# Kernel tuning notes

Measured on AMD Instinct MI355X. Metric: run time of the kernel, lower is better.

The kernel has to match this reference:

```python
import jax, jax.numpy as jnp
import numpy as np

B, SQ, HIDDEN = 2, 2048, 2048
HEADS, GROUPS, KVC = 16, 4, 128
HPG = HEADS // GROUPS          # heads per group
LAYER_INDEX = 1
SCALE = KVC ** -0.5            # attention_softmax_scale_power = 0.5


def setup_inputs() -> dict:
    key = jax.random.key(0)
    k1, k2, k3, k4 = jax.random.split(key, 4)
    return {
        "x": jax.random.normal(k1, (B, SQ, HIDDEN), jnp.float32),
        "w_q": jax.random.normal(k2, (HIDDEN, HEADS * KVC), jnp.float32) * 0.02,
        "w_kv": jax.random.normal(k3, (HIDDEN, 2 * GROUPS * KVC), jnp.float32) * 0.02,
        "w_dense": jax.random.normal(k4, (HEADS * KVC, HIDDEN), jnp.float32) * 0.02,
    }


def reference(x, w_q, w_kv, w_dense):
    b, sq, _ = x.shape
    sk = sq
    # QKV projections
    q = jnp.einsum("bsh,he->bse", x, w_q).reshape(b, sq, GROUPS, HPG, KVC)
    kv = jnp.einsum("bsh,he->bse", x, w_kv)
    k, v = jnp.split(kv, 2, axis=-1)
    k = k.reshape(b, sk, GROUPS, KVC)
    v = v.reshape(b, sk, GROUPS, KVC)
    # scaled QK^T with the per-layer scale trick: alpha = scale/L in input
    # dtype, then cast to fp32 and multiply by L (as in _attn_fused)
    scores = jnp.einsum("bqgpd,bkgd->bgqpk", q, k) * (SCALE / LAYER_INDEX)
    scores = scores.astype(jnp.float32) * LAYER_INDEX
    # causal mask: mask = ~triu(ones, diagonal=1) -> keep where q_idx >= k_idx
    causal = (jnp.arange(sq)[:, None] >= jnp.arange(sk)[None, :])
    scores = jnp.where(causal[None, None, :, None, :], scores, -jnp.inf)
    probs = jax.nn.softmax(scores, axis=-1).astype(x.dtype)
    # dropout p = 0.0 -> no-op
    ctx = jnp.einsum("bgqpk,bkgd->bqgpd", probs, v).reshape(b, sq, HEADS * KVC)
    return jnp.einsum("bse,eh->bsh", ctx, w_dense)
```

## Files before the change

### kernel.cpp

```cpp
#include <hip/hip_runtime.h>
#include <hip/hip_bf16.h>


typedef __attribute__((ext_vector_type(4))) float f32x4;
typedef __attribute__((ext_vector_type(8))) short bf16x8;
typedef __attribute__((ext_vector_type(4))) short bf16x4;

__device__ __forceinline__ unsigned short f2bf(float f) {
    unsigned u = __builtin_bit_cast(unsigned, f);
    unsigned r = u + 0x7fffu + ((u >> 16) & 1u);
    return (unsigned short)(r >> 16);
}

__device__ __forceinline__ unsigned cvtpk_bf16(float lo, float hi) {
    unsigned r;
    asm("v_cvt_pk_bf16_f32 %0, %1, %2" : "=v"(r) : "v"(lo), "v"(hi));
    return r;
}

__device__ __forceinline__ void gl_lds16(const void* g, void* l) {
    __builtin_amdgcn_global_load_lds(
        (const __attribute__((address_space(1))) unsigned int*)g,
        (__attribute__((address_space(3))) unsigned int*)l, 16, 0, 0);
}

__global__ __launch_bounds__(256)
void xcvt_kernel(const float* __restrict__ in, unsigned short* __restrict__ out)
{
    size_t i = ((size_t)blockIdx.x * 256 + threadIdx.x) * 8;
    float4 a = *reinterpret_cast<const float4*>(&in[i]);
    float4 b = *reinterpret_cast<const float4*>(&in[i + 4]);
    bf16x8 o = { (short)f2bf(a.x), (short)f2bf(a.y),
                 (short)f2bf(a.z), (short)f2bf(a.w),
                 (short)f2bf(b.x), (short)f2bf(b.y),
                 (short)f2bf(b.z), (short)f2bf(b.w) };
    *reinterpret_cast<bf16x8*>(&out[i]) = o;
}

__global__ __launch_bounds__(256)
void wtrans_kernel(const float* __restrict__ in, unsigned short* __restrict__ out,
                   int K, int N)
{
    __shared__ unsigned short T[64][72];
    const int n0 = blockIdx.x * 64, k0 = blockIdx.y * 64;
    const int tid = threadIdx.x;
#pragma unroll
    for (int i = 0; i < 4; ++i) {
        int f = tid + i * 256;
        int r = f >> 4;
        int c4 = (f & 15) * 4;
        float4 v = *reinterpret_cast<const float4*>(&in[(size_t)(k0 + r) * N + n0 + c4]);
        bf16x4 pk = { (short)f2bf(v.x), (short)f2bf(v.y),
                      (short)f2bf(v.z), (short)f2bf(v.w) };
        *reinterpret_cast<bf16x4*>(&T[r][c4]) = pk;
    }
    __syncthreads();
#pragma unroll
    for (int i = 0; i < 2; ++i) {
        int f = tid + i * 256;
        int nn = f >> 3;
        int s8 = (f & 7) * 8;
        bf16x8 o;
#pragma unroll
        for (int j = 0; j < 8; ++j) o[j] = T[s8 + j][nn];
        *reinterpret_cast<bf16x8*>(&out[(size_t)(n0 + nn) * K + k0 + s8]) = o;
    }
}

template<bool SPLIT_QKV>
__global__ __launch_bounds__(256)
void gemm_bt_kernel(const unsigned short* __restrict__ A,
                    const unsigned short* __restrict__ BT,
                    void* __restrict__ C0v, void* __restrict__ C1v,
                    int M, int N, int K)
{
    __shared__ __align__(16) unsigned short Alds[2][128 * 64];
    __shared__ __align__(16) unsigned short Blds[2][128 * 64];

    const int tid = threadIdx.x;
    const int lane = tid & 63;
    const int wid = tid >> 6;
    const int wr = wid >> 1, wc = wid & 1;
    const int m0 = blockIdx.y * 128;
    const int n0 = blockIdx.x * 128;
    const int l16 = lane & 15, lg = lane >> 4;

    f32x4 acc[4][4];
#pragma unroll
    for (int m = 0; m < 4; ++m)
#pragma unroll
        for (int n = 0; n < 4; ++n) acc[m][n] = (f32x4){0.f, 0.f, 0.f, 0.f};

    auto stage = [&](int kt, int bi) {
#pragma unroll
        for (int i = 0; i < 4; ++i) {
            int row = i * 32 + (tid >> 3);
            int cb = ((tid & 7) * 16) ^ ((row & 7) << 4);
            gl_lds16((const char*)A + ((size_t)(m0 + row) * K + kt) * 2 + cb,
                     (char*)(&Alds[bi][0]) + i * 4096 + wid * 1024);
            gl_lds16((const char*)BT + ((size_t)(n0 + row) * K + kt) * 2 + cb,
                     (char*)(&Blds[bi][0]) + i * 4096 + wid * 1024);
        }
    };

    const int NK = K / 64;
    stage(0, 0);
    int cur = 0;

    for (int kti = 0; kti < NK; ++kti) {
        if (kti + 1 < NK) {
            stage((kti + 1) * 64, cur ^ 1);
            asm volatile("s_waitcnt vmcnt(8)" ::: "memory");
        } else {
            asm volatile("s_waitcnt vmcnt(0)" ::: "memory");
        }
        __builtin_amdgcn_s_barrier();

        const char* Ab = (const char*)(&Alds[cur][0]);
        const char* Bb = (const char*)(&Blds[cur][0]);

        bf16x8 af[2][4], bf[2][4];
#pragma unroll
        for (int kd = 0; kd < 2; ++kd) {
#pragma unroll
            for (int m = 0; m < 4; ++m) {
                int row = wr * 64 + m * 16 + l16;
                af[kd][m] = *reinterpret_cast<const bf16x8*>(
                    Ab + row * 128 + ((kd * 64 + lg * 16) ^ ((row & 7) << 4)));
            }
#pragma unroll
            for (int n = 0; n < 4; ++n) {
                int row = wc * 64 + n * 16 + l16;
                bf[kd][n] = *reinterpret_cast<const bf16x8*>(
                    Bb + row * 128 + ((kd * 64 + lg * 16) ^ ((row & 7) << 4)));
            }
        }
#pragma unroll
        for (int kd = 0; kd < 2; ++kd)
#pragma unroll
            for (int m = 0; m < 4; ++m)
#pragma unroll
                for (int n = 0; n < 4; ++n)
                    acc[m][n] = __builtin_amdgcn_mfma_f32_16x16x32_bf16(
                        af[kd][m], bf[kd][n], acc[m][n], 0, 0, 0);

        __builtin_amdgcn_s_barrier();
        cur ^= 1;
    }

#pragma unroll
    for (int m = 0; m < 4; ++m) {
#pragma unroll
        for (int n = 0; n < 4; ++n) {
#pragma unroll
            for (int r = 0; r < 4; ++r) {
                int row = m0 + wr * 64 + m * 16 + lg * 4 + r;
                int col = n0 + wc * 64 + n * 16 + l16;
                float val = acc[m][n][r];
                if constexpr (SPLIT_QKV) {
                    if (n0 < 2048)
                        ((unsigned short*)C0v)[(size_t)row * 2048 + col] =
                            f2bf(val * 0.12751879523209208f);
                    else
                        ((unsigned short*)C1v)[(size_t)row * 1024 + (col - 2048)] = f2bf(val);
                } else {
                    ((float*)C0v)[(size_t)row * N + col] = val;
                }
            }
        }
    }
}

__global__ __launch_bounds__(256)
void vtrans_kernel(const unsigned short* __restrict__ kv,
                   unsigned short* __restrict__ vt)
{
    __shared__ unsigned short T[64][140];
    const int bg = blockIdx.y;
    const int b = bg >> 2, g = bg & 3;
    const int s0 = blockIdx.x * 64;
    const int tid = threadIdx.x;

#pragma unroll
    for (int i = 0; i < 4; ++i) {
        int f = tid + i * 256;
        int sl = f >> 4;
        int d0 = (f & 15) * 8;
        bf16x8 v = *reinterpret_cast<const bf16x8*>(
            &kv[(size_t)(b * 2048 + s0 + sl) * 1024 + 512 + g * 128 + d0]);
        bf16x4 lo = { v[0], v[1], v[2], v[3] };
        bf16x4 hi = { v[4], v[5], v[6], v[7] };
        *reinterpret_cast<bf16x4*>(&T[sl][d0])     = lo;
        *reinterpret_cast<bf16x4*>(&T[sl][d0 + 4]) = hi;
    }
    __syncthreads();
#pragma unroll
    for (int i = 0; i < 4; ++i) {
        int f = tid + i * 256;
        int d = f >> 3;
        int s8 = (f & 7) * 8;
        bf16x8 o;
#pragma unroll
        for (int j = 0; j < 8; ++j) o[j] = T[s8 + j][d];
        *reinterpret_cast<bf16x8*>(
            &vt[(size_t)(bg * 128 + d) * 2048 + s0 + s8]) = o;
    }
}

__global__ __launch_bounds__(256)
void attn_kernel(const unsigned short* __restrict__ Q,
                 const unsigned short* __restrict__ KV,
                 const unsigned short* __restrict__ VT,
                 unsigned short* __restrict__ CTX)
{
    constexpr int SQ = 2048;
    __shared__ __align__(16) unsigned short Klds[2][64 * 128];
    __shared__ __align__(16) unsigned short Vlds[2][128 * 64];
    __shared__ __align__(16) unsigned short Pl[4][16][64];

    const int tid = threadIdx.x;
    const int lane = tid & 63;
    const int w = tid >> 6;
    const int l16 = lane & 15, lg = lane >> 4;

    const int bid = blockIdx.x;
    const int gb = bid & 7;
    const int g = gb & 3, b = gb >> 2;
    const int pi = bid >> 3;
    const int hh = g * 4 + w;

    const size_t qbase = (size_t)b * SQ * 2048;
    const char* KVb = (const char*)KV + (size_t)b * SQ * 2048;
    const char* VTb = (const char*)VT;

    const int pswz = (l16 & 7) << 3;

    auto stage = [&](int t, int bi) {
        const int k0 = t * 64;
#pragma unroll
        for (int i = 0; i < 4; ++i) {
            int row = w * 16 + i * 4 + (lane >> 4);
            int scol = ((lane & 15) * 16) ^ ((row & 7) << 4);
            gl_lds16(KVb + (size_t)(k0 + row) * 2048 + g * 256 + scol,
                     (char*)(&Klds[bi][0]) + w * 4096 + i * 1024);
        }
#pragma unroll
        for (int i = 0; i < 4; ++i) {
            int row = w * 32 + i * 8 + (lane >> 3);
            int scol = ((lane & 7) * 16) ^ ((row & 7) << 4);
            gl_lds16(VTb + ((size_t)(gb * 128 + row) * 2048 + k0) * 2 + scol,
                     (char*)(&Vlds[bi][0]) + w * 4096 + i * 1024);
        }
    };

#pragma unroll 1
    for (int seg = 0; seg < 2; ++seg) {
        const int qt = seg ? pi : (127 - pi);
        const int ntiles = qt / 4 + 1;

        bf16x8 qfrag[4];
#pragma unroll
        for (int kd = 0; kd < 4; ++kd)
            qfrag[kd] = *reinterpret_cast<const bf16x8*>(
                &Q[qbase + (size_t)(qt * 16 + l16) * 2048 + hh * 128 + kd * 32 + lg * 8]);

        float lsum = 0.f;
        f32x4 acc[8];
#pragma unroll
        for (int nd = 0; nd < 8; ++nd) acc[nd] = (f32x4){0.f,0.f,0.f,0.f};

        stage(0, 0);

        for (int t = 0; t < ntiles; ++t) {
            const int bi = t & 1;
            const int k0 = t * 64;
            if (t + 1 < ntiles) {
                stage(t + 1, bi ^ 1);
                asm volatile("s_waitcnt vmcnt(8)" ::: "memory");
            } else {
                asm volatile("s_waitcnt vmcnt(0)" ::: "memory");
            }
            __builtin_amdgcn_s_barrier();

            const char* Kb = (const char*)(&Klds[bi][0]);
            const char* Vb = (const char*)(&Vlds[bi][0]);

            f32x4 st[4];
#pragma unroll
            for (int nf = 0; nf < 4; ++nf) st[nf] = (f32x4){0.f,0.f,0.f,0.f};
            __builtin_amdgcn_s_setprio(1);
#pragma unroll
            for (int nf = 0; nf < 4; ++nf) {
                int row = nf * 16 + l16;
#pragma unroll
                for (int kd = 0; kd < 4; ++kd) {
                    bf16x8 kf = *reinterpret_cast<const bf16x8*>(
                        Kb + row * 256 + ((kd * 64 + lg * 16) ^ ((row & 7) << 4)));
                    st[nf] = __builtin_amdgcn_mfma_f32_16x16x32_bf16(
                        kf, qfrag[kd], st[nf], 0, 0, 0);
                }
            }
            __builtin_amdgcn_s_setprio(0);

            const bool diag = (t == ntiles - 1);
            {
                float lacc = 0.f;
                const int q = qt * 16 + l16;
#pragma unroll
                for (int nf = 0; nf < 4; ++nf) {
                    float cs0 = st[nf][0];
                    float cs1 = st[nf][1];
                    float cs2 = st[nf][2];
                    float cs3 = st[nf][3];
                    if (diag) {
                        const int keyb = k0 + nf * 16 + lg * 4;
                        if (keyb + 0 > q) cs0 = -INFINITY;
                        if (keyb + 1 > q) cs1 = -INFINITY;
                        if (keyb + 2 > q) cs2 = -INFINITY;
                        if (keyb + 3 > q) cs3 = -INFINITY;
                    }
                    float p0 = exp2f(cs0), p1 = exp2f(cs1);
                    float p2 = exp2f(cs2), p3 = exp2f(cs3);
                    lacc += (p0 + p1) + (p2 + p3);
                    uint2 pk = { cvtpk_bf16(p0, p1), cvtpk_bf16(p2, p3) };
                    *reinterpret_cast<uint2*>(
                        &Pl[w][l16][(nf * 16 + lg * 4) ^ pswz]) = pk;
                }
                lacc += __shfl_xor(lacc, 16, 64);
                lacc += __shfl_xor(lacc, 32, 64);
                lsum += lacc;
            }

            __builtin_amdgcn_s_setprio(1);
#pragma unroll
            for (int kc = 0; kc < 2; ++kc) {
                bf16x8 pf = *reinterpret_cast<const bf16x8*>(
                    &Pl[w][l16][(kc * 32 + lg * 8) ^ pswz]);
#pragma unroll
                for (int nd = 0; nd < 8; ++nd) {
                    int row = nd * 16 + l16;
                    bf16x8 vf = *reinterpret_cast<const bf16x8*>(
                        Vb + row * 128 + ((kc * 64 + lg * 16) ^ ((row & 7) << 4)));
                    acc[nd] = __builtin_amdgcn_mfma_f32_16x16x32_bf16(
                        vf, pf, acc[nd], 0, 0, 0);
                }
            }
            __builtin_amdgcn_s_setprio(0);
            __builtin_amdgcn_s_barrier();
        }

        {
            float inv = 1.0f / lsum;
            const int q = qt * 16 + l16;
#pragma unroll
            for (int nd = 0; nd < 8; ++nd) {
                bf16x4 o = { (short)f2bf(acc[nd][0] * inv),
                             (short)f2bf(acc[nd][1] * inv),
                             (short)f2bf(acc[nd][2] * inv),
                             (short)f2bf(acc[nd][3] * inv) };
                *reinterpret_cast<bf16x4*>(
                    &CTX[qbase + (size_t)q * 2048 + hh * 128 + nd * 16 + lg * 4]) = o;
            }
        }
    }
}

extern "C" void kernel_launch(void* const* d_in, const int* in_sizes, int n_in,
                              void* d_out, int out_size, void* d_ws, size_t ws_size,
                              hipStream_t stream)
{
    const float* x       = (const float*)d_in[0];
    const float* w_q     = (const float*)d_in[1];
    const float* w_kv    = (const float*)d_in[2];
    const float* w_dense = (const float*)d_in[3];

    const int M = 4096;

    char* ws = (char*)d_ws;
    unsigned short* kv_buf  = (unsigned short*)(ws);
    unsigned short* ctx_buf = (unsigned short*)(ws + (8u << 20));
    unsigned short* wqT     = (unsigned short*)(ws + (24u << 20));
    unsigned short* wkvT    = (unsigned short*)(ws + (32u << 20));
    unsigned short* wdT     = wqT;
    unsigned short* xbf    = (unsigned short*)d_out;
    unsigned short* q_buf  = (unsigned short*)d_out + (size_t)M * 2048;
    unsigned short* vt_buf = (unsigned short*)d_out;

    dim3 blk(256);
    xcvt_kernel<<<dim3(4096), blk, 0, stream>>>(x, xbf);
    wtrans_kernel<<<dim3(32, 32), blk, 0, stream>>>(w_q, wqT, 2048, 2048);
    wtrans_kernel<<<dim3(16, 32), blk, 0, stream>>>(w_kv, wkvT, 2048, 1024);
    gemm_bt_kernel<true><<<dim3(24, 32), blk, 0, stream>>>(
        xbf, wqT, (void*)q_buf, (void*)kv_buf, M, 3072, 2048);
    wtrans_kernel<<<dim3(32, 32), blk, 0, stream>>>(w_dense, wdT, 2048, 2048);
    vtrans_kernel<<<dim3(32, 8), blk, 0, stream>>>(kv_buf, vt_buf);
    attn_kernel<<<dim3(512), blk, 0, stream>>>(q_buf, kv_buf, vt_buf, ctx_buf);
    gemm_bt_kernel<false><<<dim3(16, 32), blk, 0, stream>>>(
        ctx_buf, wdT, d_out, nullptr, M, 2048, 2048);
}
```

Baseline: 198.3 us.

## Use triple-buffered K=32 LDS pipeline for QKV projection GEMM

```diff
diff --git a/kernel.cpp b/kernel.cpp
--- a/kernel.cpp
+++ b/kernel.cpp
@@ -67,15 +67,14 @@
     }
 }
 
-template<bool SPLIT_QKV>
-__global__ __launch_bounds__(256)
-void gemm_bt_kernel(const unsigned short* __restrict__ A,
-                    const unsigned short* __restrict__ BT,
-                    void* __restrict__ C0v, void* __restrict__ C1v,
-                    int M, int N, int K)
-{
-    __shared__ __align__(16) unsigned short Alds[2][128 * 64];
-    __shared__ __align__(16) unsigned short Blds[2][128 * 64];
+__global__ __launch_bounds__(256)
+void gemm_qkv_kernel(const unsigned short* __restrict__ A,
+                     const unsigned short* __restrict__ BT,
+                     void* __restrict__ C0v, void* __restrict__ C1v,
+                     int M, int N, int K)
+{
+    __shared__ __align__(16) unsigned short Alds[3][128 * 32];
+    __shared__ __align__(16) unsigned short Blds[3][128 * 32];
 
     const int tid = threadIdx.x;
     const int lane = tid & 63;
@@ -91,6 +90,112 @@
 #pragma unroll
         for (int n = 0; n < 4; ++n) acc[m][n] = (f32x4){0.f, 0.f, 0.f, 0.f};
 
+    int srow[2], skb[2];
+#pragma unroll
+    for (int i = 0; i < 2; ++i) {
+        int L = i * 4096 + tid * 16;
+        int R = L >> 7, c = L & 127;
+        int cp = c ^ ((R & 7) << 4);
+        srow[i] = 2 * R + (cp >> 6);
+        skb[i]  = cp & 63;
+    }
+
+    auto stage = [&](int kt, int bi) {
+#pragma unroll
+        for (int i = 0; i < 2; ++i) {
+            int L = i * 4096 + tid * 16;
+            gl_lds16((const char*)A + ((size_t)(m0 + srow[i]) * K + kt) * 2 + skb[i],
+                     (char*)(&Alds[bi][0]) + L);
+            gl_lds16((const char*)BT + ((size_t)(n0 + srow[i]) * K + kt) * 2 + skb[i],
+                     (char*)(&Blds[bi][0]) + L);
+        }
+    };
+
+    const int NK = K / 32;
+    stage(0, 0);
+    stage(32, 1);
+
+    for (int t = 0; t < NK; ++t) {
+        const int bi = t % 3;
+        if (t + 2 < NK) {
+            stage((t + 2) * 32, (t + 2) % 3);
+            asm volatile("s_waitcnt vmcnt(8)" ::: "memory");
+        } else if (t + 1 < NK) {
+            asm volatile("s_waitcnt vmcnt(4)" ::: "memory");
+        } else {
+            asm volatile("s_waitcnt vmcnt(0)" ::: "memory");
+        }
+        __builtin_amdgcn_s_barrier();
+
+        const char* Ab = (const char*)(&Alds[bi][0]);
+        const char* Bb = (const char*)(&Blds[bi][0]);
+
+        bf16x8 af[4], bf[4];
+#pragma unroll
+        for (int m = 0; m < 4; ++m) {
+            int row = wr * 64 + m * 16 + l16;
+            int byte = (row >> 1) * 128 +
+                       ((((row & 1) << 6) + lg * 16) ^ (((row >> 1) & 7) << 4));
+            af[m] = *reinterpret_cast<const bf16x8*>(Ab + byte);
+        }
+#pragma unroll
+        for (int n = 0; n < 4; ++n) {
+            int row = wc * 64 + n * 16 + l16;
+            int byte = (row >> 1) * 128 +
+                       ((((row & 1) << 6) + lg * 16) ^ (((row >> 1) & 7) << 4));
+            bf[n] = *reinterpret_cast<const bf16x8*>(Bb + byte);
+        }
+#pragma unroll
+        for (int m = 0; m < 4; ++m)
+#pragma unroll
+            for (int n = 0; n < 4; ++n)
+                acc[m][n] = __builtin_amdgcn_mfma_f32_16x16x32_bf16(
+                    af[m], bf[n], acc[m][n], 0, 0, 0);
+
+        __builtin_amdgcn_s_barrier();
+    }
+
+#pragma unroll
+    for (int m = 0; m < 4; ++m) {
+#pragma unroll
+        for (int n = 0; n < 4; ++n) {
+#pragma unroll
+            for (int r = 0; r < 4; ++r) {
+                int row = m0 + wr * 64 + m * 16 + lg * 4 + r;
+                int col = n0 + wc * 64 + n * 16 + l16;
+                float val = acc[m][n][r];
+                if (n0 < 2048)
+                    ((unsigned short*)C0v)[(size_t)row * 2048 + col] =
+                        f2bf(val * 0.12751879523209208f);
+                else
+                    ((unsigned short*)C1v)[(size_t)row * 1024 + (col - 2048)] = f2bf(val);
+            }
+        }
+    }
+}
+
+__global__ __launch_bounds__(256)
+void gemm_dense_kernel(const unsigned short* __restrict__ A,
+                       const unsigned short* __restrict__ BT,
+                       float* __restrict__ C, int M, int N, int K)
+{
+    __shared__ __align__(16) unsigned short Alds[2][128 * 64];
+    __shared__ __align__(16) unsigned short Blds[2][128 * 64];
+
+    const int tid = threadIdx.x;
+    const int lane = tid & 63;
+    const int wid = tid >> 6;
+    const int wr = wid >> 1, wc = wid & 1;
+    const int m0 = blockIdx.y * 128;
+    const int n0 = blockIdx.x * 128;
+    const int l16 = lane & 15, lg = lane >> 4;
+
+    f32x4 acc[4][4];
+#pragma unroll
+    for (int m = 0; m < 4; ++m)
+#pragma unroll
+        for (int n = 0; n < 4; ++n) acc[m][n] = (f32x4){0.f, 0.f, 0.f, 0.f};
+
     auto stage = [&](int kt, int bi) {
 #pragma unroll
         for (int i = 0; i < 4; ++i) {
@@ -156,16 +261,7 @@
             for (int r = 0; r < 4; ++r) {
                 int row = m0 + wr * 64 + m * 16 + lg * 4 + r;
                 int col = n0 + wc * 64 + n * 16 + l16;
-                float val = acc[m][n][r];
-                if constexpr (SPLIT_QKV) {
-                    if (n0 < 2048)
-                        ((unsigned short*)C0v)[(size_t)row * 2048 + col] =
-                            f2bf(val * 0.12751879523209208f);
-                    else
-                        ((unsigned short*)C1v)[(size_t)row * 1024 + (col - 2048)] = f2bf(val);
-                } else {
-                    ((float*)C0v)[(size_t)row * N + col] = val;
-                }
+                C[(size_t)row * N + col] = acc[m][n][r];
             }
         }
     }
@@ -390,11 +486,11 @@
     xcvt_kernel<<<dim3(4096), blk, 0, stream>>>(x, xbf);
     wtrans_kernel<<<dim3(32, 32), blk, 0, stream>>>(w_q, wqT, 2048, 2048);
     wtrans_kernel<<<dim3(16, 32), blk, 0, stream>>>(w_kv, wkvT, 2048, 1024);
-    gemm_bt_kernel<true><<<dim3(24, 32), blk, 0, stream>>>(
+    gemm_qkv_kernel<<<dim3(24, 32), blk, 0, stream>>>(
         xbf, wqT, (void*)q_buf, (void*)kv_buf, M, 3072, 2048);
     wtrans_kernel<<<dim3(32, 32), blk, 0, stream>>>(w_dense, wdT, 2048, 2048);
     vtrans_kernel<<<dim3(32, 8), blk, 0, stream>>>(kv_buf, vt_buf);
     attn_kernel<<<dim3(512), blk, 0, stream>>>(q_buf, kv_buf, vt_buf, ctx_buf);
-    gemm_bt_kernel<false><<<dim3(16, 32), blk, 0, stream>>>(
-        ctx_buf, wdT, d_out, nullptr, M, 2048, 2048);
-}
+    gemm_dense_kernel<<<dim3(16, 32), blk, 0, stream>>>(
+        ctx_buf, wdT, (float*)d_out, M, 2048, 2048);
+}
```

Measured after the change: 190.5 us. 1.04x faster.
